# Kernel tuning notes

Measured on AMD Instinct MI355X. Metric: run time of the kernel, lower is better.

## Reference

```python
import jax, jax.numpy as jnp
import numpy as np
import math
from jax import lax

B, D, L, K, CONV_NUM, NH, DK = 8, 128, 1024, 7, 4, 8, 16


def _pos_encoding():
    i = np.arange(D, dtype=np.float64)
    freqs = np.where(i % 2 == 0, 10000.0 ** (-i / D), -(10000.0 ** (-(i - 1) / D)))
    phases = np.where(i % 2 == 0, 0.0, math.pi / 2)
    pos = np.arange(L, dtype=np.float64)
    pe = np.sin(pos[None, :] * freqs[:, None] + phases[:, None])  # [D, L]
    return jnp.asarray(pe, dtype=jnp.float32)


def setup_inputs() -> dict:
    key = jax.random.key(0)
    ks = jax.random.split(key, 10)
    x = jax.random.normal(ks[0], (B, D, L), dtype=jnp.float32)
    pos_enc = _pos_encoding()
    ln_w = jnp.ones((D, L), dtype=jnp.float32)   # LayerNorm([D, L]) weight
    ln_b = jnp.zeros((D, L), dtype=jnp.float32)  # LayerNorm([D, L]) bias
    dw = jax.random.normal(ks[1], (CONV_NUM, D, K), dtype=jnp.float32) * 0.1   # depthwise kernels
    pw = jax.random.normal(ks[2], (CONV_NUM, D, D), dtype=jnp.float32) * 0.08  # pointwise (1x1) kernels
    Wq = jax.random.normal(ks[3], (NH, B, DK, D), dtype=jnp.float32) * 0.08
    Wk = jax.random.normal(ks[4], (NH, B, DK, D), dtype=jnp.float32) * 0.08
    Wv = jax.random.normal(ks[5], (NH, B, DK, D), dtype=jnp.float32) * 0.08
    Wo = jax.random.normal(ks[6], (B, D, D), dtype=jnp.float32) * 0.08
    W = jax.random.normal(ks[7], (B, D, D), dtype=jnp.float32) * 0.08
    return {"x": x, "pos_enc": pos_enc, "ln_w": ln_w, "ln_b": ln_b,
            "dw": dw, "pw": pw, "Wq": Wq, "Wk": Wk, "Wv": Wv, "Wo": Wo, "W": W}


def _layernorm(y, w, b):
    # normalized over the last two dims [D, L] (matches nn.LayerNorm([D, L]))
    m = jnp.mean(y, axis=(1, 2), keepdims=True)
    v = jnp.var(y, axis=(1, 2), keepdims=True)
    return (y - m) / jnp.sqrt(v + 1e-5) * w + b


def _dsconv(y, dwk, pwk):
    # depthwise conv1d (groups=D, padding=K//2, no bias), then pointwise 1x1
    y = lax.conv_general_dilated(
        y, dwk[:, None, :], window_strides=(1,), padding=[(K // 2, K // 2)],
        feature_group_count=D, dimension_numbers=("NCH", "OIH", "NCH"))
    return jnp.einsum("oc,bcl->bol", pwk, y)


def _self_attention(x, Wq, Wk, Wv, Wo):
    inv = 1.0 / math.sqrt(DK)
    Q = jnp.einsum("hbdc,bcl->hbdl", Wq, x)  # [NH,B,DK,L]
    Kt = jnp.einsum("hbdc,bcl->hbdl", Wk, x)
    V = jnp.einsum("hbdc,bcl->hbdl", Wv, x)
    scores = jnp.einsum("hbdl,hbdm->hblm", Q, Kt) * inv  # [NH,B,L,L]
    # torch does F.softmax(out, dim=1) on [B,L,L] -> softmax over the first L axis
    A = jax.nn.softmax(scores, axis=2)
    heads = jnp.einsum("hbvl,hblm->hbvm", V, A)  # [NH,B,DV,L]
    head = jnp.transpose(heads, (1, 0, 2, 3)).reshape(B, NH * DK, L)  # concat along channel dim
    return jnp.einsum("bdc,bcl->bdl", Wo, head)


def reference(x, pos_enc, ln_w, ln_b, dw, pw, Wq, Wk, Wv, Wo, W):
    # dropout layers are identity (eval mode)
    out = x + pos_enc[None, :, :]
    res = out
    for i in range(CONV_NUM):
        out = _layernorm(out, ln_w, ln_b)
        out = _dsconv(out, dw[i], pw[i])
        out = jax.nn.relu(out)
        out = out + res
        res = out
        out = _layernorm(out, ln_w, ln_b)
    out = _self_attention(out, Wq, Wk, Wv, Wo)
    out = out + res
    res = out
    out = _layernorm(out, ln_w, ln_b)
    out = jnp.einsum("bdc,bcl->bdl", W, out)
    out = jax.nn.relu(out)
    out = out + res
    return out
```

## Files before the change

### kernel.cpp

```cpp
#include <hip/hip_runtime.h>
#include <hip/hip_bf16.h>

#define B_ 8
#define D_ 128
#define L_ 1024
#define KSZ 7
#define NH_ 8
#define DK_ 16

constexpr int BD = D_ * L_;
constexpr float LN_EPS = 1e-5f;
constexpr float INV_N = 1.0f / (float)BD;

typedef _Float16 half4 __attribute__((ext_vector_type(4)));
typedef _Float16 half8 __attribute__((ext_vector_type(8)));
typedef float f32x4 __attribute__((ext_vector_type(4)));

template<int NS>
__device__ __forceinline__ void block_reduce_wave(float* s, float* redbuf, float* slot, int tid) {
    #pragma unroll
    for (int k = 0; k < NS; ++k) {
        float v = s[k];
        #pragma unroll
        for (int mk = 32; mk >= 1; mk >>= 1) v += __shfl_xor(v, mk, 64);
        s[k] = v;
    }
    int w = tid >> 6, lane = tid & 63;
    __syncthreads();
    if (lane == 0) {
        #pragma unroll
        for (int k = 0; k < NS; ++k) redbuf[w * NS + k] = s[k];
    }
    __syncthreads();
    if (tid == 0) {
        #pragma unroll
        for (int k = 0; k < NS; ++k)
            slot[k] = redbuf[k] + redbuf[NS + k] + redbuf[2 * NS + k] + redbuf[3 * NS + k];
    }
}

template<int LNMODE>
__device__ __forceinline__ void ln_stats_wave0(
    const float* __restrict__ pin, const float* __restrict__ wmom,
    int b, float* stat4, int tid)
{
    if (tid < 64) {
        float s0=0,s1=0,s2=0,s3=0,s4=0,s5=0,w0=0,w1=0,w2=0,w3=0,w4=0;
        const float* p = pin + (b * 64 + tid) * 8;
        s0 = p[0]; s1 = p[1];
        if constexpr (LNMODE == 2) {
            s2 = p[2]; s3 = p[3]; s4 = p[4]; s5 = p[5];
            const float* q = wmom + tid * 8;
            w0 = q[0]; w1 = q[1]; w2 = q[2]; w3 = q[3]; w4 = q[4];
        }
        #pragma unroll
        for (int mk = 32; mk >= 1; mk >>= 1) {
            s0 += __shfl_xor(s0, mk, 64); s1 += __shfl_xor(s1, mk, 64);
            if constexpr (LNMODE == 2) {
                s2 += __shfl_xor(s2, mk, 64); s3 += __shfl_xor(s3, mk, 64);
                s4 += __shfl_xor(s4, mk, 64); s5 += __shfl_xor(s5, mk, 64);
                w0 += __shfl_xor(w0, mk, 64); w1 += __shfl_xor(w1, mk, 64);
                w2 += __shfl_xor(w2, mk, 64); w3 += __shfl_xor(w3, mk, 64);
                w4 += __shfl_xor(w4, mk, 64);
            }
        }
        if (tid == 0) {
            float m1 = s0 * INV_N;
            float r1 = rsqrtf(s1 * INV_N - m1 * m1 + LN_EPS);
            stat4[0] = m1; stat4[1] = r1;
            if constexpr (LNMODE == 2) {
                float Sy  = r1 * (s2 - m1 * w0) + w2;
                float Sy2 = r1 * r1 * (s4 - 2.f * m1 * s3 + m1 * m1 * w1)
                          + 2.f * r1 * (s5 - m1 * w4) + w3;
                float m2 = Sy * INV_N;
                float r2 = rsqrtf(Sy2 * INV_N - m2 * m2 + LN_EPS);
                stat4[2] = m2; stat4[3] = r2;
            }
        }
    }
    __syncthreads();
}

__global__ __launch_bounds__(256) void k_addpos_wm(
    const float* __restrict__ x, const float* __restrict__ pos,
    const float* __restrict__ lnw, const float* __restrict__ lnb,
    float* __restrict__ out, float* __restrict__ part, float* __restrict__ wp)
{
    __shared__ float red[32];
    int b = blockIdx.y, blk = blockIdx.x, tid = threadIdx.x;
    if (b == 8) {
        int base = blk * 2048 + tid * 8;
        float s[5] = {0.f, 0.f, 0.f, 0.f, 0.f};
        #pragma unroll
        for (int q = 0; q < 2; ++q) {
            float4 wv = *(const float4*)(lnw + base + q * 4);
            float4 bv = *(const float4*)(lnb + base + q * 4);
            float wa[4] = {wv.x, wv.y, wv.z, wv.w};
            float ba[4] = {bv.x, bv.y, bv.z, bv.w};
            #pragma unroll
            for (int e = 0; e < 4; ++e) {
                float w = wa[e], bb = ba[e];
                s[0] += w; s[1] += w * w; s[2] += bb; s[3] += bb * bb; s[4] += w * bb;
            }
        }
        block_reduce_wave<5>(s, red, wp + blk * 8, tid);
        return;
    }
    int base = b * BD + blk * 2048;
    const float4* x4 = (const float4*)(x + base);
    const float4* p4 = (const float4*)(pos + blk * 2048);
    float4* o4 = (float4*)(out + base);
    float s[2] = {0.f, 0.f};
    #pragma unroll
    for (int j = 0; j < 2; ++j) {
        int idx = j * 256 + tid;
        float4 xv = x4[idx], pv = p4[idx];
        float4 r = {xv.x + pv.x, xv.y + pv.y, xv.z + pv.z, xv.w + pv.w};
        o4[idx] = r;
        s[0] += r.x + r.y + r.z + r.w;
        s[1] += r.x * r.x + r.y * r.y + r.z * r.z + r.w * r.w;
    }
    block_reduce_wave<2>(s, red, part + (b * 64 + blk) * 8, tid);
}

template<int LNMODE>
__global__ __launch_bounds__(256) void k_convblock(
    const float* __restrict__ src, const float* __restrict__ lnw, const float* __restrict__ lnb,
    const float* __restrict__ dwk, const float* __restrict__ pwk,
    const float* __restrict__ wmom, const float* __restrict__ pin,
    float* __restrict__ outbuf, float* __restrict__ pout)
{
    constexpr int XSTR = 136;
    constexpr int CSTR = 20;
    __shared__ _Float16 Xt[16 * XSTR];
    __shared__ float Ct[128 * CSTR];
    __shared__ float stat4[4];
    __shared__ float red[32];
    int lt = blockIdx.x, b = blockIdx.y;
    int tid = threadIdx.x;
    int l0 = lt * 16;

    ln_stats_wave0<LNMODE>(pin, wmom, b, stat4, tid);
    float m1 = stat4[0], r1 = stat4[1];
    float m2 = 0.f, r2 = 1.f;
    if constexpr (LNMODE == 2) { m2 = stat4[2]; r2 = stat4[3]; }

    {
        int c = tid >> 1, lh = tid & 1;
        int base = l0 + lh * 8;
        const float* srow = src + b * BD + c * L_;
        const float* wrow = lnw + c * L_;
        const float* brow = lnb + c * L_;
        float z[16];
        #pragma unroll
        for (int q = 0; q < 4; ++q) {
            int le = base - 4 + q * 4;
            if (le >= 0 && le <= L_ - 4) {
                float4 sv = *(const float4*)(srow + le);
                float4 wv = *(const float4*)(wrow + le);
                float4 bv = *(const float4*)(brow + le);
                float sa[4] = {sv.x, sv.y, sv.z, sv.w};
                float wa[4] = {wv.x, wv.y, wv.z, wv.w};
                float ba[4] = {bv.x, bv.y, bv.z, bv.w};
                #pragma unroll
                for (int e = 0; e < 4; ++e) {
                    float y = (sa[e] - m1) * r1 * wa[e] + ba[e];
                    if constexpr (LNMODE == 2) y = (y - m2) * r2 * wa[e] + ba[e];
                    z[q * 4 + e] = y;
                }
            } else {
                #pragma unroll
                for (int e = 0; e < 4; ++e) {
                    int l = le + e;
                    float zz = 0.f;
                    if (l >= 0 && l < L_) {
                        float y = (srow[l] - m1) * r1 * wrow[l] + brow[l];
                        if constexpr (LNMODE == 2) y = (y - m2) * r2 * wrow[l] + brow[l];
                        zz = y;
                    }
                    z[q * 4 + e] = zz;
                }
            }
        }
        float t0 = dwk[c*KSZ+0], t1 = dwk[c*KSZ+1], t2 = dwk[c*KSZ+2], t3 = dwk[c*KSZ+3],
              t4 = dwk[c*KSZ+4], t5 = dwk[c*KSZ+5], t6 = dwk[c*KSZ+6];
        #pragma unroll
        for (int j = 0; j < 8; ++j) {
            float o = t0*z[j+1] + t1*z[j+2] + t2*z[j+3] + t3*z[j+4]
                    + t4*z[j+5] + t5*z[j+6] + t6*z[j+7];
            Xt[(lh * 8 + j) * XSTR + c] = (_Float16)o;
        }
    }
    __syncthreads();

    int w = tid >> 6, lane = tid & 63, lg = lane >> 4, ln = lane & 15;
    int o0 = w * 32;
    const float* wrow0 = pwk + (o0 + ln) * D_;
    const float* wrow1 = pwk + (o0 + 16 + ln) * D_;
    f32x4 acc0 = {0.f, 0.f, 0.f, 0.f};
    f32x4 acc1 = {0.f, 0.f, 0.f, 0.f};
    #pragma unroll
    for (int kk = 0; kk < 8; ++kk) {
        float4 wv0 = *(const float4*)(wrow0 + kk * 16 + lg * 4);
        float4 wv1 = *(const float4*)(wrow1 + kk * 16 + lg * 4);
        half4 af0 = {(_Float16)wv0.x, (_Float16)wv0.y, (_Float16)wv0.z, (_Float16)wv0.w};
        half4 af1 = {(_Float16)wv1.x, (_Float16)wv1.y, (_Float16)wv1.z, (_Float16)wv1.w};
        half4 bf = *(const half4*)(&Xt[ln * XSTR + kk * 16 + lg * 4]);
        acc0 = __builtin_amdgcn_mfma_f32_16x16x16f16(af0, bf, acc0, 0, 0, 0);
        acc1 = __builtin_amdgcn_mfma_f32_16x16x16f16(af1, bf, acc1, 0, 0, 0);
    }

    #pragma unroll
    for (int om = 0; om < 2; ++om) {
        const f32x4& a = om ? acc1 : acc0;
        #pragma unroll
        for (int r = 0; r < 4; ++r)
            Ct[(o0 + om * 16 + lg * 4 + r) * CSTR + ln] = a[r];
    }
    __syncthreads();

    float s[6] = {0.f, 0.f, 0.f, 0.f, 0.f, 0.f};
    {
        int og = tid >> 1, hh = tid & 1;
        int lcol = l0 + hh * 8;
        int idx = b * BD + og * L_ + lcol;
        int widx = og * L_ + lcol;
        float4 c0 = *(const float4*)(&Ct[og * CSTR + hh * 8]);
        float4 c1 = *(const float4*)(&Ct[og * CSTR + hh * 8 + 4]);
        float4 rs0 = *(const float4*)(src + idx);
        float4 rs1 = *(const float4*)(src + idx + 4);
        float4 w0 = *(const float4*)(lnw + widx);
        float4 w1 = *(const float4*)(lnw + widx + 4);
        float4 b0 = *(const float4*)(lnb + widx);
        float4 b1 = *(const float4*)(lnb + widx + 4);
        float cv[8] = {c0.x, c0.y, c0.z, c0.w, c1.x, c1.y, c1.z, c1.w};
        float rv[8] = {rs0.x, rs0.y, rs0.z, rs0.w, rs1.x, rs1.y, rs1.z, rs1.w};
        float wv[8] = {w0.x, w0.y, w0.z, w0.w, w1.x, w1.y, w1.z, w1.w};
        float bv[8] = {b0.x, b0.y, b0.z, b0.w, b1.x, b1.y, b1.z, b1.w};
        float ov[8];
        #pragma unroll
        for (int e = 0; e < 8; ++e) {
            float v = fmaxf(cv[e], 0.f) + rv[e];
            ov[e] = v;
            float wvv = wv[e] * v;
            s[0] += v; s[1] += v * v; s[2] += wvv;
            s[3] += wv[e] * wvv; s[4] += wvv * wvv; s[5] += bv[e] * wvv;
        }
        *(float4*)(outbuf + idx)     = (float4){ov[0], ov[1], ov[2], ov[3]};
        *(float4*)(outbuf + idx + 4) = (float4){ov[4], ov[5], ov[6], ov[7]};
    }
    block_reduce_wave<6>(s, red, pout + (b * 64 + lt) * 8, tid);
}

template<bool LNSTAGE, int XSTR>
__device__ __forceinline__ void stage_tile(
    const float* __restrict__ X, const float* __restrict__ lnw, const float* __restrict__ lnb,
    _Float16* Xt, int b, int l0, float m1, float r1, int tid)
{
    int c = tid >> 1, lh = tid & 1;
    int off = c * L_ + l0 + lh * 16;
    const float* xp = X + b * BD + off;
    const float* wp = lnw + off;
    const float* bp = lnb + off;
    #pragma unroll
    for (int q = 0; q < 4; ++q) {
        float4 v = *(const float4*)(xp + q * 4);
        if constexpr (LNSTAGE) {
            float4 wv = *(const float4*)(wp + q * 4);
            float4 bv = *(const float4*)(bp + q * 4);
            v.x = (v.x - m1) * r1 * wv.x + bv.x;
            v.y = (v.y - m1) * r1 * wv.y + bv.y;
            v.z = (v.z - m1) * r1 * wv.z + bv.z;
            v.w = (v.w - m1) * r1 * wv.w + bv.w;
        }
        int lb_ = lh * 16 + q * 4;
        Xt[(lb_ + 0) * XSTR + c] = (_Float16)v.x;
        Xt[(lb_ + 1) * XSTR + c] = (_Float16)v.y;
        Xt[(lb_ + 2) * XSTR + c] = (_Float16)v.z;
        Xt[(lb_ + 3) * XSTR + c] = (_Float16)v.w;
    }
}

__global__ __launch_bounds__(256) void k_qkv(
    const float* __restrict__ Wq, const float* __restrict__ Wk, const float* __restrict__ Wv,
    const float* __restrict__ X, const float* __restrict__ lnw, const float* __restrict__ lnb,
    const float* __restrict__ pin,
    _Float16* __restrict__ Qt, _Float16* __restrict__ Kt, _Float16* __restrict__ Vh)
{
    constexpr int XSTR = 136;
    constexpr int CSTR = 36;
    __shared__ _Float16 Xt[32 * XSTR];
    __shared__ float Ct[64 * CSTR];
    __shared__ float stat4[4];
    int lt = blockIdx.x, rb = blockIdx.y, b = blockIdx.z;
    int tid = threadIdx.x;
    int l0 = lt * 32, r0 = rb * 64;

    ln_stats_wave0<1>(pin, nullptr, b, stat4, tid);
    stage_tile<true, XSTR>(X, lnw, lnb, Xt, b, l0, stat4[0], stat4[1], tid);
    __syncthreads();

    int w = tid >> 6, lane = tid & 63, lg = lane >> 4, ln = lane & 15;
    int o = r0 + w * 16 + ln;
    int woff = (o >> 4) * (B_ * DK_ * D_) + b * (DK_ * D_) + (o & 15) * D_;

    half4 bf[2][8];
    #pragma unroll
    for (int n = 0; n < 2; ++n)
        #pragma unroll
        for (int kk = 0; kk < 8; ++kk)
            bf[n][kk] = *(const half4*)(&Xt[(n * 16 + ln) * XSTR + kk * 16 + lg * 4]);

    const float* Wms[3] = {Wq, Wk, Wv};
    #pragma unroll
    for (int g = 0; g < 3; ++g) {
        const float* wrow = Wms[g] + woff;
        f32x4 acc0 = {0.f, 0.f, 0.f, 0.f};
        f32x4 acc1 = {0.f, 0.f, 0.f, 0.f};
        #pragma unroll
        for (int kk = 0; kk < 8; ++kk) {
            float4 wv = *(const float4*)(wrow + kk * 16 + lg * 4);
            half4 af = {(_Float16)wv.x, (_Float16)wv.y, (_Float16)wv.z, (_Float16)wv.w};
            acc0 = __builtin_amdgcn_mfma_f32_16x16x16f16(af, bf[0][kk], acc0, 0, 0, 0);
            acc1 = __builtin_amdgcn_mfma_f32_16x16x16f16(af, bf[1][kk], acc1, 0, 0, 0);
        }
        if (g) __syncthreads();
        #pragma unroll
        for (int n = 0; n < 2; ++n) {
            const f32x4& a = n ? acc1 : acc0;
            #pragma unroll
            for (int r = 0; r < 4; ++r)
                Ct[(w * 16 + lg * 4 + r) * CSTR + n * 16 + ln] = a[r];
        }
        __syncthreads();
        if (g < 2) {
            int hd = tid >> 6, lrel = (tid >> 1) & 31, hf = tid & 1;
            int h = rb * 4 + hd, l = l0 + lrel;
            half8 hv;
            #pragma unroll
            for (int k = 0; k < 8; ++k)
                hv[k] = (_Float16)Ct[(hd * 16 + hf * 8 + k) * CSTR + lrel];
            _Float16* dst = (g == 0 ? Qt : Kt);
            *(half8*)(dst + ((b * NH_ + h) * L_ + l) * 16 + hf * 8) = hv;
        } else {
            int row = tid >> 2, q4 = tid & 3;
            int h = rb * 4 + (row >> 4), v = row & 15;
            float4 c0 = *(const float4*)(&Ct[row * CSTR + q4 * 8]);
            float4 c1 = *(const float4*)(&Ct[row * CSTR + q4 * 8 + 4]);
            half8 hv = {(_Float16)c0.x, (_Float16)c0.y, (_Float16)c0.z, (_Float16)c0.w,
                        (_Float16)c1.x, (_Float16)c1.y, (_Float16)c1.z, (_Float16)c1.w};
            *(half8*)(Vh + ((b * NH_ + h) * DK_ + v) * L_ + l0 + q4 * 8) = hv;
        }
    }
}

__global__ __launch_bounds__(256) void k_attn_mfma(
    const _Float16* __restrict__ Qt, const _Float16* __restrict__ Kt,
    const _Float16* __restrict__ Vh, _Float16* __restrict__ H16)
{
    constexpr int VSTR = 72;
    __shared__ _Float16 Vs[2][16 * VSTR];
    __shared__ _Float16 Om[64 * 16];
    int mt = blockIdx.x, h = blockIdx.y, b = blockIdx.z;
    int tid = threadIdx.x;
    int w = tid >> 6, lane = tid & 63, lg = lane >> 4, ln = lane & 15;
    int m = mt * 64 + w * 16 + ln;
    const _Float16* Qh = Qt + (b * NH_ + h) * L_ * 16;
    const _Float16* Kh = Kt + (b * NH_ + h) * L_ * 16;
    const _Float16* Vp = Vh + (b * NH_ + h) * DK_ * L_;

    half4 kraw = *(const half4*)(Kh + m * 16 + lg * 4);
    half4 kfrag;
    #pragma unroll
    for (int j = 0; j < 4; ++j) kfrag[j] = kraw[j] * (_Float16)0.25f;

    f32x4 accf[4];
    #pragma unroll
    for (int f = 0; f < 4; ++f) accf[f] = (f32x4){0.f, 0.f, 0.f, 0.f};
    float run_sm = 0.f;

    int sv = tid >> 4, sq = tid & 15;
    const _Float16* vsrc = Vp + sv * L_ + sq * 4;
    half4 vreg = *(const half4*)(vsrc);

    for (int lt = 0; lt < 16; ++lt) {
        int cb = lt & 1;
        int l0 = lt * 64;
        *(half4*)(&Vs[cb][sv * VSTR + sq * 4]) = vreg;
        __syncthreads();
        if (lt < 15) vreg = *(const half4*)(vsrc + (lt + 1) * 64);

        f32x4 s[4];
        #pragma unroll
        for (int f = 0; f < 4; ++f) {
            half4 qf = *(const half4*)(Qh + (l0 + f * 16 + ln) * 16 + lg * 4);
            f32x4 z = {0.f, 0.f, 0.f, 0.f};
            s[f] = __builtin_amdgcn_mfma_f32_16x16x16f16(qf, kfrag, z, 0, 0, 0);
        }

        float ts = 0.f;
        half4 pf[4];
        #pragma unroll
        for (int f = 0; f < 4; ++f) {
            float p0 = __expf(s[f][0]);
            float p1 = __expf(s[f][1]);
            float p2 = __expf(s[f][2]);
            float p3 = __expf(s[f][3]);
            ts += (p0 + p1) + (p2 + p3);
            pf[f][0] = (_Float16)p0; pf[f][1] = (_Float16)p1;
            pf[f][2] = (_Float16)p2; pf[f][3] = (_Float16)p3;
        }
        ts += __shfl_xor(ts, 16, 64);
        ts += __shfl_xor(ts, 32, 64);
        run_sm += ts;

        #pragma unroll
        for (int f = 0; f < 4; ++f) {
            half4 vf = *(const half4*)(&Vs[cb][ln * VSTR + f * 16 + lg * 4]);
            accf[f] = __builtin_amdgcn_mfma_f32_16x16x16f16(vf, pf[f], accf[f], 0, 0, 0);
        }
    }

    float inv = 1.f / run_sm;
    #pragma unroll
    for (int r = 0; r < 4; ++r) {
        float a = (accf[0][r] + accf[1][r]) + (accf[2][r] + accf[3][r]);
        Om[(w * 16 + ln) * 16 + lg * 4 + r] = (_Float16)(a * inv);
    }
    __syncthreads();
    if (tid < 128) {
        int ml = tid >> 1, hf = tid & 1;
        half8 hv = *(const half8*)(&Om[ml * 16 + hf * 8]);
        *(half8*)(H16 + (b * L_ + mt * 64 + ml) * 128 + h * 16 + hf * 8) = hv;
    }
}

__global__ __launch_bounds__(256) void k_matmul_h16(
    const float* __restrict__ Wm, const _Float16* __restrict__ H16,
    const float* __restrict__ res, float* __restrict__ out, float* __restrict__ part)
{
    constexpr int HSTR = 136;
    constexpr int CSTR = 36;
    __shared__ _Float16 Xh[32 * HSTR];
    __shared__ float Ct[64 * CSTR];
    __shared__ float red[32];
    int lt = blockIdx.x, rb = blockIdx.y, b = blockIdx.z;
    int tid = threadIdx.x;
    int l0 = lt * 32, r0 = rb * 64;
    const _Float16* Hb = H16 + (size_t)b * L_ * 128;

    {
        int l = tid >> 3, seg = tid & 7;
        const _Float16* src = Hb + (l0 + l) * 128 + seg * 16;
        *(half8*)(&Xh[l * HSTR + seg * 16])     = *(const half8*)(src);
        *(half8*)(&Xh[l * HSTR + seg * 16 + 8]) = *(const half8*)(src + 8);
    }
    __syncthreads();

    int w = tid >> 6, lane = tid & 63, lg = lane >> 4, ln = lane & 15;
    int o = r0 + w * 16 + ln;
    const float* wrow = Wm + b * D_ * D_ + o * D_;

    f32x4 acc0 = {0.f, 0.f, 0.f, 0.f};
    f32x4 acc1 = {0.f, 0.f, 0.f, 0.f};
    #pragma unroll
    for (int kk = 0; kk < 8; ++kk) {
        float4 wv = *(const float4*)(wrow + kk * 16 + lg * 4);
        half4 af = {(_Float16)wv.x, (_Float16)wv.y, (_Float16)wv.z, (_Float16)wv.w};
        half4 b0 = *(const half4*)(&Xh[ln * HSTR + kk * 16 + lg * 4]);
        half4 b1 = *(const half4*)(&Xh[(16 + ln) * HSTR + kk * 16 + lg * 4]);
        acc0 = __builtin_amdgcn_mfma_f32_16x16x16f16(af, b0, acc0, 0, 0, 0);
        acc1 = __builtin_amdgcn_mfma_f32_16x16x16f16(af, b1, acc1, 0, 0, 0);
    }

    #pragma unroll
    for (int n = 0; n < 2; ++n) {
        const f32x4& a = n ? acc1 : acc0;
        #pragma unroll
        for (int r = 0; r < 4; ++r)
            Ct[(w * 16 + lg * 4 + r) * CSTR + n * 16 + ln] = a[r];
    }
    __syncthreads();

    float s[2] = {0.f, 0.f};
    {
        int row = tid >> 2, q4 = tid & 3;
        int og = r0 + row, lcol = l0 + q4 * 8;
        int idx = b * BD + og * L_ + lcol;
        float4 c0 = *(const float4*)(&Ct[row * CSTR + q4 * 8]);
        float4 c1 = *(const float4*)(&Ct[row * CSTR + q4 * 8 + 4]);
        float4 r0v = *(const float4*)(res + idx);
        float4 r1v = *(const float4*)(res + idx + 4);
        float cv[8] = {c0.x, c0.y, c0.z, c0.w, c1.x, c1.y, c1.z, c1.w};
        float rv[8] = {r0v.x, r0v.y, r0v.z, r0v.w, r1v.x, r1v.y, r1v.z, r1v.w};
        float ov[8];
        #pragma unroll
        for (int e = 0; e < 8; ++e) {
            float v = cv[e] + rv[e];
            ov[e] = v;
            s[0] += v; s[1] += v * v;
        }
        *(float4*)(out + idx)     = (float4){ov[0], ov[1], ov[2], ov[3]};
        *(float4*)(out + idx + 4) = (float4){ov[4], ov[5], ov[6], ov[7]};
    }
    block_reduce_wave<2>(s, red, part + (b * 64 + rb * 32 + lt) * 8, tid);
}

template<bool RELU, bool ADDRES, bool STATS, bool LNSTAGE>
__global__ __launch_bounds__(256) void k_matmul_mfma(
    const float* __restrict__ Wm, const float* __restrict__ X,
    const float* __restrict__ lnw, const float* __restrict__ lnb,
    const float* __restrict__ pin,
    const float* __restrict__ res, float* __restrict__ out, float* __restrict__ part)
{
    constexpr int XSTR = 136;
    constexpr int CSTR = 36;
    __shared__ _Float16 Xt[32 * XSTR];
    __shared__ float Ct[64 * CSTR];
    __shared__ float stat4[4];
    __shared__ float red[32];
    int lt = blockIdx.x, rb = blockIdx.y, b = blockIdx.z;
    int tid = threadIdx.x;
    int l0 = lt * 32, r0 = rb * 64;

    if constexpr (LNSTAGE) ln_stats_wave0<1>(pin, nullptr, b, stat4, tid);
    float m1 = LNSTAGE ? stat4[0] : 0.f, r1 = LNSTAGE ? stat4[1] : 1.f;
    stage_tile<LNSTAGE, XSTR>(X, lnw, lnb, Xt, b, l0, m1, r1, tid);
    __syncthreads();

    int w = tid >> 6, lane = tid & 63, lg = lane >> 4, ln = lane & 15;
    int o = r0 + w * 16 + ln;
    const float* wrow = Wm + b * D_ * D_ + o * D_;

    f32x4 acc0 = {0.f, 0.f, 0.f, 0.f};
    f32x4 acc1 = {0.f, 0.f, 0.f, 0.f};
    #pragma unroll
    for (int kk = 0; kk < 8; ++kk) {
        float4 wv = *(const float4*)(wrow + kk * 16 + lg * 4);
        half4 af = {(_Float16)wv.x, (_Float16)wv.y, (_Float16)wv.z, (_Float16)wv.w};
        half4 b0 = *(const half4*)(&Xt[ln * XSTR + kk * 16 + lg * 4]);
        half4 b1 = *(const half4*)(&Xt[(16 + ln) * XSTR + kk * 16 + lg * 4]);
        acc0 = __builtin_amdgcn_mfma_f32_16x16x16f16(af, b0, acc0, 0, 0, 0);
        acc1 = __builtin_amdgcn_mfma_f32_16x16x16f16(af, b1, acc1, 0, 0, 0);
    }

    #pragma unroll
    for (int n = 0; n < 2; ++n) {
        const f32x4& a = n ? acc1 : acc0;
        #pragma unroll
        for (int r = 0; r < 4; ++r)
            Ct[(w * 16 + lg * 4 + r) * CSTR + n * 16 + ln] = a[r];
    }
    __syncthreads();

    float s[2] = {0.f, 0.f};
    {
        int row = tid >> 2, q4 = tid & 3;
        int og = r0 + row, lcol = l0 + q4 * 8;
        int idx = b * BD + og * L_ + lcol;
        float4 c0 = *(const float4*)(&Ct[row * CSTR + q4 * 8]);
        float4 c1 = *(const float4*)(&Ct[row * CSTR + q4 * 8 + 4]);
        float cv[8] = {c0.x, c0.y, c0.z, c0.w, c1.x, c1.y, c1.z, c1.w};
        float rv[8] = {0.f, 0.f, 0.f, 0.f, 0.f, 0.f, 0.f, 0.f};
        if constexpr (ADDRES) {
            float4 r0v = *(const float4*)(res + idx);
            float4 r1v = *(const float4*)(res + idx + 4);
            rv[0]=r0v.x; rv[1]=r0v.y; rv[2]=r0v.z; rv[3]=r0v.w;
            rv[4]=r1v.x; rv[5]=r1v.y; rv[6]=r1v.z; rv[7]=r1v.w;
        }
        float ov[8];
        #pragma unroll
        for (int e = 0; e < 8; ++e) {
            float v = cv[e];
            if constexpr (RELU) v = fmaxf(v, 0.f);
            v += rv[e];
            ov[e] = v;
            if constexpr (STATS) { s[0] += v; s[1] += v * v; }
        }
        *(float4*)(out + idx)     = (float4){ov[0], ov[1], ov[2], ov[3]};
        *(float4*)(out + idx + 4) = (float4){ov[4], ov[5], ov[6], ov[7]};
    }
    if constexpr (STATS) block_reduce_wave<2>(s, red, part + (b * 64 + rb * 32 + lt) * 8, tid);
}


extern "C" void kernel_launch(void* const* d_in, const int* in_sizes, int n_in,
                              void* d_out, int out_size, void* d_ws, size_t ws_size,
                              hipStream_t stream)
{
    const float* x   = (const float*)d_in[0];
    const float* pos = (const float*)d_in[1];
    const float* lnw = (const float*)d_in[2];
    const float* lnb = (const float*)d_in[3];
    const float* dw  = (const float*)d_in[4];
    const float* pw  = (const float*)d_in[5];
    const float* Wq  = (const float*)d_in[6];
    const float* Wk  = (const float*)d_in[7];
    const float* Wv  = (const float*)d_in[8];
    const float* Wo  = (const float*)d_in[9];
    const float* Wf  = (const float*)d_in[10];
    float* out = (float*)d_out;

    float* ws = (float*)d_ws;
    float* WP = ws;
    float* P0 = ws + 512;
    float* P1 = P0 + 4096;
    float* P2 = P1 + 4096;
    float* P3 = P2 + 4096;
    float* P4 = P3 + 4096;
    float* P5 = P4 + 4096;
    float* bufA = ws + 32768;
    float* bufB = bufA + (size_t)B_ * BD;
    float* bufC = bufB + (size_t)B_ * BD;
    _Float16* Qt  = (_Float16*)(bufC + (size_t)B_ * BD);
    _Float16* Kt  = Qt + (size_t)B_ * NH_ * L_ * 16;
    _Float16* Vh  = Kt + (size_t)B_ * NH_ * L_ * 16;
    _Float16* H16 = Vh + (size_t)B_ * NH_ * DK_ * L_;

    dim3 cb(64, 8);
    dim3 mb(32, 2, 8);

    k_addpos_wm<<<dim3(64, 9), 256, 0, stream>>>(x, pos, lnw, lnb, bufA, P0, WP);

    k_convblock<1><<<cb, 256, 0, stream>>>(bufA, lnw, lnb, dw + 0*D_*KSZ, pw + 0*D_*D_, WP, P0, bufB, P1);
    k_convblock<2><<<cb, 256, 0, stream>>>(bufB, lnw, lnb, dw + 1*D_*KSZ, pw + 1*D_*D_, WP, P1, bufA, P2);
    k_convblock<2><<<cb, 256, 0, stream>>>(bufA, lnw, lnb, dw + 2*D_*KSZ, pw + 2*D_*D_, WP, P2, bufB, P3);
    k_convblock<2><<<cb, 256, 0, stream>>>(bufB, lnw, lnb, dw + 3*D_*KSZ, pw + 3*D_*D_, WP, P3, bufA, P4);

    k_qkv<<<mb, 256, 0, stream>>>(Wq, Wk, Wv, bufA, lnw, lnb, P4, Qt, Kt, Vh);

    k_attn_mfma<<<dim3(16, NH_, B_), 256, 0, stream>>>(Qt, Kt, Vh, H16);

    k_matmul_h16<<<mb, 256, 0, stream>>>(Wo, H16, bufA, bufC, P5);
    k_matmul_mfma<true, true, false, true><<<mb, 256, 0, stream>>>(Wf, bufC, lnw, lnb, P5, bufC, out, nullptr);
}
```

Baseline: 109.5 us.

## Split conv and final matmul blocks over output rows; write Q/K directly from MFMA

The conv-block kernel now splits output channels into two 64-row halves with an extra grid dimension, doubling the block count. The LN partial-stat reduction is generalized to 128 partials using a two-wave reduction. The final matmul uses 16-column tiles to spread work over more blocks. The QKV kernel writes Q and K straight from the MFMA accumulators, skipping the shared-memory transpose and two barriers. The trade-off is that each conv block recomputes the full depthwise conv and LN staging for all channels, doubling that input work.

```diff
diff --git a/kernel.cpp b/kernel.cpp
--- a/kernel.cpp
+++ b/kernel.cpp
@@ -39,19 +39,21 @@
     }
 }
 
-template<int LNMODE>
+template<int LNMODE, int NP>
 __device__ __forceinline__ void ln_stats_wave0(
     const float* __restrict__ pin, const float* __restrict__ wmom,
-    int b, float* stat4, int tid)
-{
-    if (tid < 64) {
+    int b, float* stat4, float* red, int tid)
+{
+    if (tid < NP) {
         float s0=0,s1=0,s2=0,s3=0,s4=0,s5=0,w0=0,w1=0,w2=0,w3=0,w4=0;
-        const float* p = pin + (b * 64 + tid) * 8;
+        const float* p = pin + (b * NP + tid) * 8;
         s0 = p[0]; s1 = p[1];
         if constexpr (LNMODE == 2) {
             s2 = p[2]; s3 = p[3]; s4 = p[4]; s5 = p[5];
-            const float* q = wmom + tid * 8;
-            w0 = q[0]; w1 = q[1]; w2 = q[2]; w3 = q[3]; w4 = q[4];
+            if (tid < 64) {
+                const float* q = wmom + tid * 8;
+                w0 = q[0]; w1 = q[1]; w2 = q[2]; w3 = q[3]; w4 = q[4];
+            }
         }
         #pragma unroll
         for (int mk = 32; mk >= 1; mk >>= 1) {
@@ -64,18 +66,38 @@
                 w4 += __shfl_xor(w4, mk, 64);
             }
         }
-        if (tid == 0) {
-            float m1 = s0 * INV_N;
-            float r1 = rsqrtf(s1 * INV_N - m1 * m1 + LN_EPS);
-            stat4[0] = m1; stat4[1] = r1;
+        if ((tid & 63) == 0) {
+            float* r = red + (tid >> 6) * 12;
+            r[0]=s0; r[1]=s1;
             if constexpr (LNMODE == 2) {
-                float Sy  = r1 * (s2 - m1 * w0) + w2;
-                float Sy2 = r1 * r1 * (s4 - 2.f * m1 * s3 + m1 * m1 * w1)
-                          + 2.f * r1 * (s5 - m1 * w4) + w3;
-                float m2 = Sy * INV_N;
-                float r2 = rsqrtf(Sy2 * INV_N - m2 * m2 + LN_EPS);
-                stat4[2] = m2; stat4[3] = r2;
-            }
+                r[2]=s2; r[3]=s3; r[4]=s4; r[5]=s5;
+                r[6]=w0; r[7]=w1; r[8]=w2; r[9]=w3; r[10]=w4;
+            }
+        }
+    }
+    __syncthreads();
+    if (tid == 0) {
+        constexpr int NW = NP / 64;
+        float s0=0,s1=0,s2=0,s3=0,s4=0,s5=0,w0=0,w1=0,w2=0,w3=0,w4=0;
+        #pragma unroll
+        for (int i = 0; i < NW; ++i) {
+            const float* r = red + i * 12;
+            s0 += r[0]; s1 += r[1];
+            if constexpr (LNMODE == 2) {
+                s2 += r[2]; s3 += r[3]; s4 += r[4]; s5 += r[5];
+                w0 += r[6]; w1 += r[7]; w2 += r[8]; w3 += r[9]; w4 += r[10];
+            }
+        }
+        float m1 = s0 * INV_N;
+        float r1 = rsqrtf(s1 * INV_N - m1 * m1 + LN_EPS);
+        stat4[0] = m1; stat4[1] = r1;
+        if constexpr (LNMODE == 2) {
+            float Sy  = r1 * (s2 - m1 * w0) + w2;
+            float Sy2 = r1 * r1 * (s4 - 2.f * m1 * s3 + m1 * m1 * w1)
+                      + 2.f * r1 * (s5 - m1 * w4) + w3;
+            float m2 = Sy * INV_N;
+            float r2 = rsqrtf(Sy2 * INV_N - m2 * m2 + LN_EPS);
+            stat4[2] = m2; stat4[3] = r2;
         }
     }
     __syncthreads();
@@ -123,7 +145,7 @@
     block_reduce_wave<2>(s, red, part + (b * 64 + blk) * 8, tid);
 }
 
-template<int LNMODE>
+template<int LNMODE, int NP>
 __global__ __launch_bounds__(256) void k_convblock(
     const float* __restrict__ src, const float* __restrict__ lnw, const float* __restrict__ lnb,
     const float* __restrict__ dwk, const float* __restrict__ pwk,
@@ -133,14 +155,14 @@
     constexpr int XSTR = 136;
     constexpr int CSTR = 20;
     __shared__ _Float16 Xt[16 * XSTR];
-    __shared__ float Ct[128 * CSTR];
+    __shared__ float Ct[64 * CSTR];
     __shared__ float stat4[4];
     __shared__ float red[32];
-    int lt = blockIdx.x, b = blockIdx.y;
+    int lt = blockIdx.x, rb = blockIdx.y, b = blockIdx.z;
     int tid = threadIdx.x;
     int l0 = lt * 16;
 
-    ln_stats_wave0<LNMODE>(pin, wmom, b, stat4, tid);
+    ln_stats_wave0<LNMODE, NP>(pin, wmom, b, stat4, red, tid);
     float m1 = stat4[0], r1 = stat4[1];
     float m2 = 0.f, r2 = 1.f;
     if constexpr (LNMODE == 2) { m2 = stat4[2]; r2 = stat4[3]; }
@@ -194,76 +216,64 @@
     __syncthreads();
 
     int w = tid >> 6, lane = tid & 63, lg = lane >> 4, ln = lane & 15;
-    int o0 = w * 32;
-    const float* wrow0 = pwk + (o0 + ln) * D_;
-    const float* wrow1 = pwk + (o0 + 16 + ln) * D_;
+    int orow = rb * 64 + w * 16;
+    const float* wrow0 = pwk + (orow + ln) * D_;
     f32x4 acc0 = {0.f, 0.f, 0.f, 0.f};
-    f32x4 acc1 = {0.f, 0.f, 0.f, 0.f};
     #pragma unroll
     for (int kk = 0; kk < 8; ++kk) {
         float4 wv0 = *(const float4*)(wrow0 + kk * 16 + lg * 4);
-        float4 wv1 = *(const float4*)(wrow1 + kk * 16 + lg * 4);
         half4 af0 = {(_Float16)wv0.x, (_Float16)wv0.y, (_Float16)wv0.z, (_Float16)wv0.w};
-        half4 af1 = {(_Float16)wv1.x, (_Float16)wv1.y, (_Float16)wv1.z, (_Float16)wv1.w};
         half4 bf = *(const half4*)(&Xt[ln * XSTR + kk * 16 + lg * 4]);
         acc0 = __builtin_amdgcn_mfma_f32_16x16x16f16(af0, bf, acc0, 0, 0, 0);
-        acc1 = __builtin_amdgcn_mfma_f32_16x16x16f16(af1, bf, acc1, 0, 0, 0);
-    }
-
-    #pragma unroll
-    for (int om = 0; om < 2; ++om) {
-        const f32x4& a = om ? acc1 : acc0;
-        #pragma unroll
-        for (int r = 0; r < 4; ++r)
-            Ct[(o0 + om * 16 + lg * 4 + r) * CSTR + ln] = a[r];
-    }
+    }
+
+    #pragma unroll
+    for (int r = 0; r < 4; ++r)
+        Ct[(w * 16 + lg * 4 + r) * CSTR + ln] = acc0[r];
     __syncthreads();
 
     float s[6] = {0.f, 0.f, 0.f, 0.f, 0.f, 0.f};
     {
-        int og = tid >> 1, hh = tid & 1;
-        int lcol = l0 + hh * 8;
+        int row = tid >> 2, q4 = tid & 3;
+        int og = rb * 64 + row;
+        int lcol = l0 + q4 * 4;
         int idx = b * BD + og * L_ + lcol;
         int widx = og * L_ + lcol;
-        float4 c0 = *(const float4*)(&Ct[og * CSTR + hh * 8]);
-        float4 c1 = *(const float4*)(&Ct[og * CSTR + hh * 8 + 4]);
-        float4 rs0 = *(const float4*)(src + idx);
-        float4 rs1 = *(const float4*)(src + idx + 4);
-        float4 w0 = *(const float4*)(lnw + widx);
-        float4 w1 = *(const float4*)(lnw + widx + 4);
-        float4 b0 = *(const float4*)(lnb + widx);
-        float4 b1 = *(const float4*)(lnb + widx + 4);
-        float cv[8] = {c0.x, c0.y, c0.z, c0.w, c1.x, c1.y, c1.z, c1.w};
-        float rv[8] = {rs0.x, rs0.y, rs0.z, rs0.w, rs1.x, rs1.y, rs1.z, rs1.w};
-        float wv[8] = {w0.x, w0.y, w0.z, w0.w, w1.x, w1.y, w1.z, w1.w};
-        float bv[8] = {b0.x, b0.y, b0.z, b0.w, b1.x, b1.y, b1.z, b1.w};
-        float ov[8];
-        #pragma unroll
-        for (int e = 0; e < 8; ++e) {
+        float4 c4 = *(const float4*)(&Ct[row * CSTR + q4 * 4]);
+        float4 rs = *(const float4*)(src + idx);
+        float4 w4 = *(const float4*)(lnw + widx);
+        float4 b4 = *(const float4*)(lnb + widx);
+        float cv[4] = {c4.x, c4.y, c4.z, c4.w};
+        float rv[4] = {rs.x, rs.y, rs.z, rs.w};
+        float wv[4] = {w4.x, w4.y, w4.z, w4.w};
+        float bv[4] = {b4.x, b4.y, b4.z, b4.w};
+        float ov[4];
+        #pragma unroll
+        for (int e = 0; e < 4; ++e) {
             float v = fmaxf(cv[e], 0.f) + rv[e];
             ov[e] = v;
             float wvv = wv[e] * v;
             s[0] += v; s[1] += v * v; s[2] += wvv;
             s[3] += wv[e] * wvv; s[4] += wvv * wvv; s[5] += bv[e] * wvv;
         }
-        *(float4*)(outbuf + idx)     = (float4){ov[0], ov[1], ov[2], ov[3]};
-        *(float4*)(outbuf + idx + 4) = (float4){ov[4], ov[5], ov[6], ov[7]};
-    }
-    block_reduce_wave<6>(s, red, pout + (b * 64 + lt) * 8, tid);
-}
-
-template<bool LNSTAGE, int XSTR>
+        *(float4*)(outbuf + idx) = (float4){ov[0], ov[1], ov[2], ov[3]};
+    }
+    block_reduce_wave<6>(s, red, pout + (b * 128 + lt * 2 + rb) * 8, tid);
+}
+
+template<bool LNSTAGE, int TL>
 __device__ __forceinline__ void stage_tile(
     const float* __restrict__ X, const float* __restrict__ lnw, const float* __restrict__ lnb,
     _Float16* Xt, int b, int l0, float m1, float r1, int tid)
 {
+    constexpr int HL = TL / 2;
     int c = tid >> 1, lh = tid & 1;
-    int off = c * L_ + l0 + lh * 16;
+    int off = c * L_ + l0 + lh * HL;
     const float* xp = X + b * BD + off;
     const float* wp = lnw + off;
     const float* bp = lnb + off;
     #pragma unroll
-    for (int q = 0; q < 4; ++q) {
+    for (int q = 0; q < HL / 4; ++q) {
         float4 v = *(const float4*)(xp + q * 4);
         if constexpr (LNSTAGE) {
             float4 wv = *(const float4*)(wp + q * 4);
@@ -273,11 +283,11 @@
             v.z = (v.z - m1) * r1 * wv.z + bv.z;
             v.w = (v.w - m1) * r1 * wv.w + bv.w;
         }
-        int lb_ = lh * 16 + q * 4;
-        Xt[(lb_ + 0) * XSTR + c] = (_Float16)v.x;
-        Xt[(lb_ + 1) * XSTR + c] = (_Float16)v.y;
-        Xt[(lb_ + 2) * XSTR + c] = (_Float16)v.z;
-        Xt[(lb_ + 3) * XSTR + c] = (_Float16)v.w;
+        int lb_ = lh * HL + q * 4;
+        Xt[(lb_ + 0) * 136 + c] = (_Float16)v.x;
+        Xt[(lb_ + 1) * 136 + c] = (_Float16)v.y;
+        Xt[(lb_ + 2) * 136 + c] = (_Float16)v.z;
+        Xt[(lb_ + 3) * 136 + c] = (_Float16)v.w;
     }
 }
 
@@ -292,12 +302,13 @@
     __shared__ _Float16 Xt[32 * XSTR];
     __shared__ float Ct[64 * CSTR];
     __shared__ float stat4[4];
+    __shared__ float red[32];
     int lt = blockIdx.x, rb = blockIdx.y, b = blockIdx.z;
     int tid = threadIdx.x;
     int l0 = lt * 32, r0 = rb * 64;
 
-    ln_stats_wave0<1>(pin, nullptr, b, stat4, tid);
-    stage_tile<true, XSTR>(X, lnw, lnb, Xt, b, l0, stat4[0], stat4[1], tid);
+    ln_stats_wave0<1, 128>(pin, nullptr, b, stat4, red, tid);
+    stage_tile<true, 32>(X, lnw, lnb, Xt, b, l0, stat4[0], stat4[1], tid);
     __syncthreads();
 
     int w = tid >> 6, lane = tid & 63, lg = lane >> 4, ln = lane & 15;
@@ -324,32 +335,32 @@
             acc0 = __builtin_amdgcn_mfma_f32_16x16x16f16(af, bf[0][kk], acc0, 0, 0, 0);
             acc1 = __builtin_amdgcn_mfma_f32_16x16x16f16(af, bf[1][kk], acc1, 0, 0, 0);
         }
-        if (g) __syncthreads();
-        #pragma unroll
-        for (int n = 0; n < 2; ++n) {
-            const f32x4& a = n ? acc1 : acc0;
+        if (g < 2) {
+            int h = rb * 4 + w;
+            _Float16* dst = (g == 0 ? Qt : Kt);
             #pragma unroll
-            for (int r = 0; r < 4; ++r)
-                Ct[(w * 16 + lg * 4 + r) * CSTR + n * 16 + ln] = a[r];
-        }
-        __syncthreads();
-        if (g < 2) {
-            int hd = tid >> 6, lrel = (tid >> 1) & 31, hf = tid & 1;
-            int h = rb * 4 + hd, l = l0 + lrel;
-            half8 hv;
+            for (int n = 0; n < 2; ++n) {
+                const f32x4& a = n ? acc1 : acc0;
+                half4 hv = {(_Float16)a[0], (_Float16)a[1], (_Float16)a[2], (_Float16)a[3]};
+                int l = l0 + n * 16 + ln;
+                *(half4*)(dst + ((size_t)(b * NH_ + h) * L_ + l) * 16 + lg * 4) = hv;
+            }
+        } else {
             #pragma unroll
-            for (int k = 0; k < 8; ++k)
-                hv[k] = (_Float16)Ct[(hd * 16 + hf * 8 + k) * CSTR + lrel];
-            _Float16* dst = (g == 0 ? Qt : Kt);
-            *(half8*)(dst + ((b * NH_ + h) * L_ + l) * 16 + hf * 8) = hv;
-        } else {
+            for (int n = 0; n < 2; ++n) {
+                const f32x4& a = n ? acc1 : acc0;
+                #pragma unroll
+                for (int r = 0; r < 4; ++r)
+                    Ct[(w * 16 + lg * 4 + r) * CSTR + n * 16 + ln] = a[r];
+            }
+            __syncthreads();
             int row = tid >> 2, q4 = tid & 3;
             int h = rb * 4 + (row >> 4), v = row & 15;
             float4 c0 = *(const float4*)(&Ct[row * CSTR + q4 * 8]);
             float4 c1 = *(const float4*)(&Ct[row * CSTR + q4 * 8 + 4]);
             half8 hv = {(_Float16)c0.x, (_Float16)c0.y, (_Float16)c0.z, (_Float16)c0.w,
                         (_Float16)c1.x, (_Float16)c1.y, (_Float16)c1.z, (_Float16)c1.w};
-            *(half8*)(Vh + ((b * NH_ + h) * DK_ + v) * L_ + l0 + q4 * 8) = hv;
+            *(half8*)(Vh + ((size_t)(b * NH_ + h) * DK_ + v) * L_ + l0 + q4 * 8) = hv;
         }
     }
 }
@@ -506,81 +517,57 @@
     block_reduce_wave<2>(s, red, part + (b * 64 + rb * 32 + lt) * 8, tid);
 }
 
-template<bool RELU, bool ADDRES, bool STATS, bool LNSTAGE>
-__global__ __launch_bounds__(256) void k_matmul_mfma(
+__global__ __launch_bounds__(256) void k_matmul_fin(
     const float* __restrict__ Wm, const float* __restrict__ X,
     const float* __restrict__ lnw, const float* __restrict__ lnb,
-    const float* __restrict__ pin,
-    const float* __restrict__ res, float* __restrict__ out, float* __restrict__ part)
+    const float* __restrict__ pin, float* __restrict__ out)
 {
     constexpr int XSTR = 136;
-    constexpr int CSTR = 36;
-    __shared__ _Float16 Xt[32 * XSTR];
+    constexpr int CSTR = 20;
+    __shared__ _Float16 Xt[16 * XSTR];
     __shared__ float Ct[64 * CSTR];
     __shared__ float stat4[4];
     __shared__ float red[32];
     int lt = blockIdx.x, rb = blockIdx.y, b = blockIdx.z;
     int tid = threadIdx.x;
-    int l0 = lt * 32, r0 = rb * 64;
-
-    if constexpr (LNSTAGE) ln_stats_wave0<1>(pin, nullptr, b, stat4, tid);
-    float m1 = LNSTAGE ? stat4[0] : 0.f, r1 = LNSTAGE ? stat4[1] : 1.f;
-    stage_tile<LNSTAGE, XSTR>(X, lnw, lnb, Xt, b, l0, m1, r1, tid);
+    int l0 = lt * 16;
+
+    ln_stats_wave0<1, 64>(pin, nullptr, b, stat4, red, tid);
+    stage_tile<true, 16>(X, lnw, lnb, Xt, b, l0, stat4[0], stat4[1], tid);
     __syncthreads();
 
     int w = tid >> 6, lane = tid & 63, lg = lane >> 4, ln = lane & 15;
-    int o = r0 + w * 16 + ln;
-    const float* wrow = Wm + b * D_ * D_ + o * D_;
+    int orow = rb * 64 + w * 16;
+    const float* wrow = Wm + b * D_ * D_ + (orow + ln) * D_;
 
     f32x4 acc0 = {0.f, 0.f, 0.f, 0.f};
-    f32x4 acc1 = {0.f, 0.f, 0.f, 0.f};
     #pragma unroll
     for (int kk = 0; kk < 8; ++kk) {
         float4 wv = *(const float4*)(wrow + kk * 16 + lg * 4);
         half4 af = {(_Float16)wv.x, (_Float16)wv.y, (_Float16)wv.z, (_Float16)wv.w};
-        half4 b0 = *(const half4*)(&Xt[ln * XSTR + kk * 16 + lg * 4]);
-        half4 b1 = *(const half4*)(&Xt[(16 + ln) * XSTR + kk * 16 + lg * 4]);
-        acc0 = __builtin_amdgcn_mfma_f32_16x16x16f16(af, b0, acc0, 0, 0, 0);
-        acc1 = __builtin_amdgcn_mfma_f32_16x16x16f16(af, b1, acc1, 0, 0, 0);
-    }
-
-    #pragma unroll
-    for (int n = 0; n < 2; ++n) {
-        const f32x4& a = n ? acc1 : acc0;
-        #pragma unroll
-        for (int r = 0; r < 4; ++r)
-            Ct[(w * 16 + lg * 4 + r) * CSTR + n * 16 + ln] = a[r];
-    }
-    __syncthreads();
-
-    float s[2] = {0.f, 0.f};
+        half4 bf = *(const half4*)(&Xt[ln * XSTR + kk * 16 + lg * 4]);
+        acc0 = __builtin_amdgcn_mfma_f32_16x16x16f16(af, bf, acc0, 0, 0, 0);
+    }
+
+    #pragma unroll
+    for (int r = 0; r < 4; ++r)
+        Ct[(w * 16 + lg * 4 + r) * CSTR + ln] = acc0[r];
+    __syncthreads();
+
     {
         int row = tid >> 2, q4 = tid & 3;
-        int og = r0 + row, lcol = l0 + q4 * 8;
+        int og = rb * 64 + row;
+        int lcol = l0 + q4 * 4;
         int idx = b * BD + og * L_ + lcol;
-        float4 c0 = *(const float4*)(&Ct[row * CSTR + q4 * 8]);
-        float4 c1 = *(const float4*)(&Ct[row * CSTR + q4 * 8 + 4]);
-        float cv[8] = {c0.x, c0.y, c0.z, c0.w, c1.x, c1.y, c1.z, c1.w};
-        float rv[8] = {0.f, 0.f, 0.f, 0.f, 0.f, 0.f, 0.f, 0.f};
-        if constexpr (ADDRES) {
-            float4 r0v = *(const float4*)(res + idx);
-            float4 r1v = *(const float4*)(res + idx + 4);
-            rv[0]=r0v.x; rv[1]=r0v.y; rv[2]=r0v.z; rv[3]=r0v.w;
-            rv[4]=r1v.x; rv[5]=r1v.y; rv[6]=r1v.z; rv[7]=r1v.w;
-        }
-        float ov[8];
-        #pragma unroll
-        for (int e = 0; e < 8; ++e) {
-            float v = cv[e];
-            if constexpr (RELU) v = fmaxf(v, 0.f);
-            v += rv[e];
-            ov[e] = v;
-            if constexpr (STATS) { s[0] += v; s[1] += v * v; }
-        }
-        *(float4*)(out + idx)     = (float4){ov[0], ov[1], ov[2], ov[3]};
-        *(float4*)(out + idx + 4) = (float4){ov[4], ov[5], ov[6], ov[7]};
-    }
-    if constexpr (STATS) block_reduce_wave<2>(s, red, part + (b * 64 + rb * 32 + lt) * 8, tid);
+        float4 c4 = *(const float4*)(&Ct[row * CSTR + q4 * 4]);
+        float4 r4 = *(const float4*)(X + idx);
+        float ov[4];
+        ov[0] = fmaxf(c4.x, 0.f) + r4.x;
+        ov[1] = fmaxf(c4.y, 0.f) + r4.y;
+        ov[2] = fmaxf(c4.z, 0.f) + r4.z;
+        ov[3] = fmaxf(c4.w, 0.f) + r4.w;
+        *(float4*)(out + idx) = (float4){ov[0], ov[1], ov[2], ov[3]};
+    }
 }
 
 
@@ -605,11 +592,11 @@
     float* WP = ws;
     float* P0 = ws + 512;
     float* P1 = P0 + 4096;
-    float* P2 = P1 + 4096;
-    float* P3 = P2 + 4096;
-    float* P4 = P3 + 4096;
-    float* P5 = P4 + 4096;
-    float* bufA = ws + 32768;
+    float* P2 = P1 + 8192;
+    float* P3 = P2 + 8192;
+    float* P4 = P3 + 8192;
+    float* P5 = P4 + 8192;
+    float* bufA = ws + 65536;
     float* bufB = bufA + (size_t)B_ * BD;
     float* bufC = bufB + (size_t)B_ * BD;
     _Float16* Qt  = (_Float16*)(bufC + (size_t)B_ * BD);
@@ -617,20 +604,21 @@
     _Float16* Vh  = Kt + (size_t)B_ * NH_ * L_ * 16;
     _Float16* H16 = Vh + (size_t)B_ * NH_ * DK_ * L_;
 
-    dim3 cb(64, 8);
-    dim3 mb(32, 2, 8);
+    dim3 cb(64, 2, 8);
+    dim3 mbq(32, 2, 8);
+    dim3 mbf(64, 2, 8);
 
     k_addpos_wm<<<dim3(64, 9), 256, 0, stream>>>(x, pos, lnw, lnb, bufA, P0, WP);
 
-    k_convblock<1><<<cb, 256, 0, stream>>>(bufA, lnw, lnb, dw + 0*D_*KSZ, pw + 0*D_*D_, WP, P0, bufB, P1);
-    k_convblock<2><<<cb, 256, 0, stream>>>(bufB, lnw, lnb, dw + 1*D_*KSZ, pw + 1*D_*D_, WP, P1, bufA, P2);
-    k_convblock<2><<<cb, 256, 0, stream>>>(bufA, lnw, lnb, dw + 2*D_*KSZ, pw + 2*D_*D_, WP, P2, bufB, P3);
-    k_convblock<2><<<cb, 256, 0, stream>>>(bufB, lnw, lnb, dw + 3*D_*KSZ, pw + 3*D_*D_, WP, P3, bufA, P4);
-
-    k_qkv<<<mb, 256, 0, stream>>>(Wq, Wk, Wv, bufA, lnw, lnb, P4, Qt, Kt, Vh);
+    k_convblock<1, 64><<<cb, 256, 0, stream>>>(bufA, lnw, lnb, dw + 0*D_*KSZ, pw + 0*D_*D_, WP, P0, bufB, P1);
+    k_convblock<2, 128><<<cb, 256, 0, stream>>>(bufB, lnw, lnb, dw + 1*D_*KSZ, pw + 1*D_*D_, WP, P1, bufA, P2);
+    k_convblock<2, 128><<<cb, 256, 0, stream>>>(bufA, lnw, lnb, dw + 2*D_*KSZ, pw + 2*D_*D_, WP, P2, bufB, P3);
+    k_convblock<2, 128><<<cb, 256, 0, stream>>>(bufB, lnw, lnb, dw + 3*D_*KSZ, pw + 3*D_*D_, WP, P3, bufA, P4);
+
+    k_qkv<<<mbq, 256, 0, stream>>>(Wq, Wk, Wv, bufA, lnw, lnb, P4, Qt, Kt, Vh);
 
     k_attn_mfma<<<dim3(16, NH_, B_), 256, 0, stream>>>(Qt, Kt, Vh, H16);
 
-    k_matmul_h16<<<mb, 256, 0, stream>>>(Wo, H16, bufA, bufC, P5);
-    k_matmul_mfma<true, true, false, true><<<mb, 256, 0, stream>>>(Wf, bufC, lnw, lnb, P5, bufC, out, nullptr);
-}
+    k_matmul_h16<<<mbq, 256, 0, stream>>>(Wo, H16, bufA, bufC, P5);
+    k_matmul_fin<<<mbf, 256, 0, stream>>>(Wf, bufC, lnw, lnb, P5, out);
+}
```

After: 122.6 us. 11.9% more time.
